# Performance work log

Measured on AMD Instinct MI355X. Metric: run time of the kernel, lower is better.

The kernel has to match this reference:

```python
import jax, jax.numpy as jnp
import numpy as np


def setup_inputs() -> dict:
    key = jax.random.key(0)
    ks = jax.random.split(key, 5)
    B, S, D, F = 4, 2048, 1024, 4096
    scale_w1 = 1.0 / np.sqrt(D)
    scale_w2 = 1.0 / np.sqrt(F)
    return {
        "hidden_states": jax.random.normal(ks[0], (B, S, D), dtype=jnp.float32),
        "W1": jax.random.normal(ks[1], (F, D), dtype=jnp.float32) * scale_w1,
        "b1": jax.random.normal(ks[2], (F,), dtype=jnp.float32) * 0.02,
        "W2": jax.random.normal(ks[3], (D, F), dtype=jnp.float32) * scale_w2,
        "b2": jax.random.normal(ks[4], (D,), dtype=jnp.float32) * 0.02,
    }


def _sigmoid_poly(h):
    # cubic polynomial sigmoid approximation: 0.5 + 0.25*h - 0.0208*h^3
    h2 = h * h
    h3 = h2 * h
    return 0.5 + 0.25 * h + (-0.0208) * h3


def reference(hidden_states, W1, b1, W2, b2):
    # secure linear projection == plain affine: x @ W.T + b
    h = jnp.einsum("bsd,fd->bsf", hidden_states, W1) + b1  # [B,S,F]
    sw = h * _sigmoid_poly(h)                               # swish via poly sigmoid
    out = jnp.einsum("bsf,df->bsd", sw, W2) + b2            # [B,S,D]
    return out
```

## Files before the change

kernel.cpp:

```cpp
#include <hip/hip_runtime.h>
#include <hip/hip_bf16.h>

typedef __bf16 bf16_t;
typedef __bf16 bf16x8 __attribute__((ext_vector_type(8)));
typedef float f32x4 __attribute__((ext_vector_type(4)));

typedef const __attribute__((address_space(3))) bf16_t* lds_cptr;

__global__ __launch_bounds__(256) void cast3_f32_to_bf16(
    const float* __restrict__ a, bf16_t* __restrict__ ao, int na8,
    const float* __restrict__ b, bf16_t* __restrict__ bo, int nb8,
    const float* __restrict__ c, bf16_t* __restrict__ co, int nc8) {
  int i = blockIdx.x * blockDim.x + threadIdx.x;
  const float* in;
  bf16_t* out;
  int j;
  if (i < na8) {
    in = a; out = ao; j = i;
  } else if (i < na8 + nb8) {
    in = b; out = bo; j = i - na8;
  } else if (i < na8 + nb8 + nc8) {
    in = c; out = co; j = i - na8 - nb8;
  } else {
    return;
  }
  const float4* in4 = (const float4*)in;
  float4 f0 = in4[2 * j];
  float4 f1 = in4[2 * j + 1];
  bf16x8 o;
  o[0] = (bf16_t)f0.x; o[1] = (bf16_t)f0.y;
  o[2] = (bf16_t)f0.z; o[3] = (bf16_t)f0.w;
  o[4] = (bf16_t)f1.x; o[5] = (bf16_t)f1.y;
  o[6] = (bf16_t)f1.z; o[7] = (bf16_t)f1.w;
  ((bf16x8*)out)[j] = o;
}

__device__ __forceinline__ void gload_lds16(const bf16_t* g, bf16_t* l) {
  __builtin_amdgcn_global_load_lds(
      (const __attribute__((address_space(1))) void*)g,
      (__attribute__((address_space(3))) void*)l,
      16, 0, 0);
}

template <int N>
__device__ __forceinline__ void vmwait() {
  if constexpr (N == 3) asm volatile("s_waitcnt vmcnt(3)");
  else if constexpr (N == 4) asm volatile("s_waitcnt vmcnt(4)");
  else asm volatile("s_waitcnt vmcnt(0)");
}

template <int I, int N, int BOFF>
__device__ __forceinline__ void ldsr_n(bf16x8* dst, lds_cptr p) {
  if constexpr (I < N) {
    asm volatile("ds_read_b128 %0, %1 offset:%2"
                 : "=v"(dst[I]) : "v"(p), "i"(BOFF + I * 1024));
    ldsr_n<I + 1, N, BOFF>(dst, p);
  }
}

#define SMALL_TILE(s_, b_, ODD_)                                              \
  {                                                                           \
    const int s__ = (s_);                                                     \
    int sw__ = s__ + 3;                                                       \
    if (sw__ >= NS) sw__ -= NS;                                               \
    lds_cptr pa3 = sA3 + (b_) * (256 * 32) + aoff;                            \
    lds_cptr pb3 = sB3 + (b_) * (BN * 32) + boff;                             \
    bf16x8 af[FRH], bq[FC];                                                   \
    ldsr_n<0, FRH, 0>(af, pa3);                                               \
    ldsr_n<0, FC, 0>(bq, pb3);                                                \
    stageA(sw__);                                                             \
    __builtin_amdgcn_s_barrier();                                             \
    asm volatile("s_waitcnt lgkmcnt(0)");                                     \
    __builtin_amdgcn_sched_barrier(0);                                        \
    __builtin_amdgcn_s_setprio(1);                                            \
    _Pragma("unroll") for (int i = 0; i < FRH; ++i)                           \
        _Pragma("unroll") for (int j = 0; j < FC; ++j)                        \
            acc[i][j] = __builtin_amdgcn_mfma_f32_16x16x32_bf16(              \
                af[i], bq[j], acc[i][j], 0, 0, 0);                            \
    __builtin_amdgcn_s_setprio(0);                                            \
    __builtin_amdgcn_s_barrier();                                             \
    bf16x8 ag[FRH];                                                           \
    ldsr_n<0, FRH, FRH * 1024>(ag, pa3);                                      \
    stageB(sw__);                                                             \
    __builtin_amdgcn_s_barrier();                                             \
    asm volatile("s_waitcnt lgkmcnt(0)");                                     \
    __builtin_amdgcn_sched_barrier(0);                                        \
    __builtin_amdgcn_s_setprio(1);                                            \
    _Pragma("unroll") for (int i = 0; i < FRH; ++i)                           \
        _Pragma("unroll") for (int j = 0; j < FC; ++j)                        \
            acc[FRH + i][j] = __builtin_amdgcn_mfma_f32_16x16x32_bf16(        \
                ag[i], bq[j], acc[FRH + i][j], 0, 0, 0);                      \
    __builtin_amdgcn_s_setprio(0);                                            \
    if (ODD_) { vmwait<VMN>(); }                                              \
    __builtin_amdgcn_s_barrier();                                             \
  }

template <int BN, int WM, int WN, bool SWISH>
__global__ __launch_bounds__(512, 2) void gemm_bt8(
    const bf16_t* __restrict__ A, const bf16_t* __restrict__ B,
    const float* __restrict__ bias, void* __restrict__ Cout,
    int M, int N, int K, int XW, int px, int py) {
  constexpr int BM = 256;
  constexpr int WR = BM / WM;
  constexpr int WC = BN / WN;
  constexpr int FR = WR / 16;
  constexpr int FC = WC / 16;
  constexpr int FRH = FR / 2;
  constexpr int ACALLS = BM / 128;
  constexpr int BCALLS = BN / 128;
  constexpr int VMN = ACALLS + BCALLS;

  const int tid = threadIdx.x;
  const int wave = tid >> 6;
  const int lane = tid & 63;

  const int bid = blockIdx.x;
  const int xcd = bid & 7;
  const int idx = bid >> 3;
  const int cx = xcd % XW;
  const int cy = xcd / XW;
  const int bx = cx * px + idx % px;
  const int by = cy * py + idx / px;
  const int tileM = by * BM;
  const int tileN = bx * BN;

  __shared__ __align__(16) bf16_t sA[4 * 256 * 32];
  __shared__ __align__(16) bf16_t sB[4 * BN * 32];
  lds_cptr sA3 = (lds_cptr)sA;
  lds_cptr sB3 = (lds_cptr)sB;

  const int srow = (wave << 4) + (lane >> 2);
  const int sgc = ((lane & 3) ^ ((lane >> 3) & 3)) << 3;
  const bf16_t* gA = A + (size_t)(tileM + srow) * K + sgc;
  const bf16_t* gB = B + (size_t)(tileN + srow) * K + sgc;
  bf16_t* lA = sA + (wave << 9);
  bf16_t* lB = sB + (wave << 9);

  auto stageA = [&](int s) {
    bf16_t* l = lA + (s & 3) * (256 * 32);
    const bf16_t* g = gA + s * 32;
#pragma unroll
    for (int c = 0; c < ACALLS; ++c)
      gload_lds16(g + (size_t)(c * 128) * K, l + c * 128 * 32);
  };
  auto stageB = [&](int s) {
    bf16_t* l = lB + (s & 3) * (BN * 32);
    const bf16_t* g = gB + s * 32;
#pragma unroll
    for (int c = 0; c < BCALLS; ++c)
      gload_lds16(g + (size_t)(c * 128) * K, l + c * 128 * 32);
  };

  const int wr = wave / WN;
  const int wc = wave % WN;
  const int fr = lane & 15;
  const int pc = (lane >> 4) ^ ((fr >> 1) & 3);
  const int aoff = (wr * WR + fr) * 32 + pc * 8;
  const int boff = (wc * WC + fr) * 32 + pc * 8;

  f32x4 acc[FR][FC] = {};

  const int NS = K >> 5;

  stageA(0); stageB(0);
  stageA(1); stageB(1);
  stageA(2); stageB(2);
  vmwait<VMN>();
  __builtin_amdgcn_s_barrier();

  for (int os = 0; os < NS; os += 4) {
    SMALL_TILE(os + 0, 0, 0)
    SMALL_TILE(os + 1, 1, 1)
    SMALL_TILE(os + 2, 2, 0)
    SMALL_TILE(os + 3, 3, 1)
  }

  const int cRow0 = tileM + wr * WR + ((lane >> 4) << 2);
  const int cCol0 = tileN + wc * WC + (lane & 15);
#pragma unroll
  for (int j = 0; j < FC; ++j) {
    const int col = cCol0 + j * 16;
    const float bv = bias[col];
#pragma unroll
    for (int i = 0; i < FR; ++i) {
      const int row = cRow0 + i * 16;
#pragma unroll
      for (int r = 0; r < 4; ++r) {
        float h = acc[i][j][r] + bv;
        if constexpr (SWISH) {
          float h3 = h * h * h;
          float sw = h * (0.5f + 0.25f * h - 0.0208f * h3);
          ((bf16_t*)Cout)[(size_t)(row + r) * N + col] = (bf16_t)sw;
        } else {
          ((float*)Cout)[(size_t)(row + r) * N + col] = h;
        }
      }
    }
  }
}

extern "C" void kernel_launch(void* const* d_in, const int* in_sizes, int n_in,
                              void* d_out, int out_size, void* d_ws,
                              size_t ws_size, hipStream_t stream) {
  const float* X  = (const float*)d_in[0];
  const float* W1 = (const float*)d_in[1];
  const float* b1 = (const float*)d_in[2];
  const float* W2 = (const float*)d_in[3];
  const float* b2 = (const float*)d_in[4];
  float* out = (float*)d_out;

  const int F = in_sizes[2];
  const int D = in_sizes[4];
  const int M = in_sizes[0] / D;

  bf16_t* Xb  = (bf16_t*)d_ws;
  bf16_t* W1b = Xb + (size_t)M * D;
  bf16_t* W2b = W1b + (size_t)F * D;
  bf16_t* SW  = W2b + (size_t)D * F;

  const int nX = (M * D) / 8, nW1 = (F * D) / 8, nW2 = (D * F) / 8;
  const int nTot = nX + nW1 + nW2;
  cast3_f32_to_bf16<<<(nTot + 255) / 256, 256, 0, stream>>>(
      X, Xb, nX, W1, W1b, nW1, W2, W2b, nW2);

  {
    const int gx = F / 256, gy = M / 256;
    const int XW = 2, XH = 4;
    const int px = gx / XW, py = gy / XH;
    gemm_bt8<256, 2, 4, true><<<gx * gy, 512, 0, stream>>>(
        Xb, W1b, b1, (void*)SW, M, F, D, XW, px, py);
  }

  {
    const int gx = D / 128, gy = M / 256;
    const int XW = 1, XH = 8;
    const int px = gx / XW, py = gy / XH;
    gemm_bt8<128, 4, 2, false><<<gx * gy, 512, 0, stream>>>(
        SW, W2b, b2, (void*)out, M, D, F, XW, px, py);
  }
}
```

Measured before the change: 265.6 us.

## Collapse two-phase K-step into single phase with per-row lgkmcnt waits

```diff
diff --git a/kernel.cpp b/kernel.cpp
--- a/kernel.cpp
+++ b/kernel.cpp
@@ -49,6 +49,11 @@
   else asm volatile("s_waitcnt vmcnt(0)");
 }
 
+template <int N>
+__device__ __forceinline__ void lgkmwait() {
+  asm volatile("s_waitcnt lgkmcnt(%0)" :: "i"(N));
+}
+
 template <int I, int N, int BOFF>
 __device__ __forceinline__ void ldsr_n(bf16x8* dst, lds_cptr p) {
   if constexpr (I < N) {
@@ -58,40 +63,35 @@
   }
 }
 
-#define SMALL_TILE(s_, b_, ODD_)                                              \
+template <int I, int FR, int FC>
+__device__ __forceinline__ void mfma_rows(const bf16x8* aq, const bf16x8* bq,
+                                          f32x4 (&acc)[FR][FC]) {
+  if constexpr (I < FR) {
+    lgkmwait<FR - 1 - I>();
+    __builtin_amdgcn_sched_barrier(0);
+#pragma unroll
+    for (int j = 0; j < FC; ++j)
+      acc[I][j] = __builtin_amdgcn_mfma_f32_16x16x32_bf16(
+          aq[I], bq[j], acc[I][j], 0, 0, 0);
+    mfma_rows<I + 1, FR, FC>(aq, bq, acc);
+  }
+}
+
+#define SMALL_TILE(s_, b_)                                                    \
   {                                                                           \
-    const int s__ = (s_);                                                     \
-    int sw__ = s__ + 3;                                                       \
+    int sw__ = (s_) + 3;                                                      \
     if (sw__ >= NS) sw__ -= NS;                                               \
     lds_cptr pa3 = sA3 + (b_) * (256 * 32) + aoff;                            \
     lds_cptr pb3 = sB3 + (b_) * (BN * 32) + boff;                             \
-    bf16x8 af[FRH], bq[FC];                                                   \
-    ldsr_n<0, FRH, 0>(af, pa3);                                               \
+    bf16x8 bq[FC], aq[FR];                                                    \
     ldsr_n<0, FC, 0>(bq, pb3);                                                \
+    ldsr_n<0, FR, 0>(aq, pa3);                                                \
     stageA(sw__);                                                             \
-    __builtin_amdgcn_s_barrier();                                             \
-    asm volatile("s_waitcnt lgkmcnt(0)");                                     \
-    __builtin_amdgcn_sched_barrier(0);                                        \
+    stageB(sw__);                                                             \
     __builtin_amdgcn_s_setprio(1);                                            \
-    _Pragma("unroll") for (int i = 0; i < FRH; ++i)                           \
-        _Pragma("unroll") for (int j = 0; j < FC; ++j)                        \
-            acc[i][j] = __builtin_amdgcn_mfma_f32_16x16x32_bf16(              \
-                af[i], bq[j], acc[i][j], 0, 0, 0);                            \
+    mfma_rows<0, FR, FC>(aq, bq, acc);                                        \
     __builtin_amdgcn_s_setprio(0);                                            \
-    __builtin_amdgcn_s_barrier();                                             \
-    bf16x8 ag[FRH];                                                           \
-    ldsr_n<0, FRH, FRH * 1024>(ag, pa3);                                      \
-    stageB(sw__);                                                             \
-    __builtin_amdgcn_s_barrier();                                             \
-    asm volatile("s_waitcnt lgkmcnt(0)");                                     \
-    __builtin_amdgcn_sched_barrier(0);                                        \
-    __builtin_amdgcn_s_setprio(1);                                            \
-    _Pragma("unroll") for (int i = 0; i < FRH; ++i)                           \
-        _Pragma("unroll") for (int j = 0; j < FC; ++j)                        \
-            acc[FRH + i][j] = __builtin_amdgcn_mfma_f32_16x16x32_bf16(        \
-                ag[i], bq[j], acc[FRH + i][j], 0, 0, 0);                      \
-    __builtin_amdgcn_s_setprio(0);                                            \
-    if (ODD_) { vmwait<VMN>(); }                                              \
+    vmwait<VMN>();                                                            \
     __builtin_amdgcn_s_barrier();                                             \
   }
 
@@ -105,7 +105,6 @@
   constexpr int WC = BN / WN;
   constexpr int FR = WR / 16;
   constexpr int FC = WC / 16;
-  constexpr int FRH = FR / 2;
   constexpr int ACALLS = BM / 128;
   constexpr int BCALLS = BN / 128;
   constexpr int VMN = ACALLS + BCALLS;
@@ -169,10 +168,10 @@
   __builtin_amdgcn_s_barrier();
 
   for (int os = 0; os < NS; os += 4) {
-    SMALL_TILE(os + 0, 0, 0)
-    SMALL_TILE(os + 1, 1, 1)
-    SMALL_TILE(os + 2, 2, 0)
-    SMALL_TILE(os + 3, 3, 1)
+    SMALL_TILE(os + 0, 0)
+    SMALL_TILE(os + 1, 1)
+    SMALL_TILE(os + 2, 2)
+    SMALL_TILE(os + 3, 3)
   }
 
   const int cRow0 = tileM + wr * WR + ((lane >> 4) << 2);
```

After: 266.6 us. No clear change (+0.4%).
